# Optimization experiments

Hardware: AMD Instinct MI355X
Metric: run time of the kernel (lower is better)

Reference implementation:

```python
import jax, jax.numpy as jnp
import numpy as np

B, CIN, COUT, K = 32, 64, 64, 128  # batch, in_channels, out_channels, kernel_size (== H == W)


def setup_inputs() -> dict:
    key = jax.random.key(0)
    k1, k2, k3, k4 = jax.random.split(key, 4)
    x = jax.random.normal(k1, (B, CIN, K, K), dtype=jnp.float32)
    # kaiming_uniform_(a=sqrt(5)) => gain=sqrt(1/3), bound = gain*sqrt(3/fan_in) = 1/sqrt(fan_in)
    fan_in = CIN * K * K
    bound = 1.0 / np.sqrt(fan_in)
    weight_real = jax.random.uniform(k2, (COUT, CIN, K, K), jnp.float32, -bound, bound)
    weight_imag = jax.random.uniform(k3, (COUT, CIN, K, K), jnp.float32, -bound, bound)
    bias = jax.random.uniform(k4, (COUT,), jnp.float32, -bound, bound)
    return {"x": x, "weight_real": weight_real, "weight_imag": weight_imag, "bias": bias}


def reference(x, weight_real, weight_imag, bias):
    # FFT over spatial dims: (B, Cin, H, W) complex
    xf = jnp.fft.fftn(x, axes=(-2, -1))
    xr, xi = jnp.real(xf), jnp.imag(xf)
    # Per-frequency complex contraction over in-channels:
    # (a+ib)(c+id) = (ac - bd) + i(ad + bc)
    conv_real = (jnp.einsum('bchw,ochw->bohw', xr, weight_real)
                 - jnp.einsum('bchw,ochw->bohw', xi, weight_imag))
    conv_imag = (jnp.einsum('bchw,ochw->bohw', xr, weight_imag)
                 + jnp.einsum('bchw,ochw->bohw', xi, weight_real))
    conv = jnp.fft.ifftn(jax.lax.complex(conv_real, conv_imag), axes=(-2, -1))
    out = jnp.real(conv) + bias[:, None, None]
    return jax.nn.relu(out)
```

## Files before the change

### kernel.cpp

```cpp
#include <hip/hip_runtime.h>
#include <hip/hip_bf16.h>
#include <math.h>


#define PI2 6.28318530717958647692f
typedef unsigned int uint32;

__device__ __forceinline__ float2 cmulf(float2 a, float2 b) {
  return make_float2(a.x * b.x - a.y * b.y, a.x * b.y + a.y * b.x);
}
__device__ __forceinline__ uint32 pack_bf(float re, float im) {
  __hip_bfloat162 h;
  h.x = __float2bfloat16(re);
  h.y = __float2bfloat16(im);
  return *(uint32*)&h;
}
__device__ __forceinline__ float2 unpack_bf(uint32 v) {
  return make_float2(__uint_as_float(v << 16), __uint_as_float(v & 0xFFFF0000u));
}
__device__ __forceinline__ int br7(int i) { return __brev((unsigned)i) >> 25; }

template <int SGN>
__device__ __forceinline__ void wave_fft128(float2& e0, float2& e1, int l) {
#pragma unroll
  for (int s = 1; s <= 6; s++) {
    const int h = 1 << (s - 1);
    const int p = l & (h - 1);
    float sn, cs;
    __sincosf((float)SGN * PI2 * (float)p / (float)(2 * h), &sn, &cs);
    const float2 w = make_float2(cs, sn);
    const bool up = (l & h) != 0;
    const float2 o0 = make_float2(__shfl_xor(e0.x, h), __shfl_xor(e0.y, h));
    const float2 o1 = make_float2(__shfl_xor(e1.x, h), __shfl_xor(e1.y, h));
    const float2 u0 = up ? o0 : e0;
    const float2 m0 = up ? e0 : o0;
    const float2 u1 = up ? o1 : e1;
    const float2 m1 = up ? e1 : o1;
    const float2 t0 = cmulf(w, m0);
    const float2 t1 = cmulf(w, m1);
    e0 = up ? make_float2(u0.x - t0.x, u0.y - t0.y) : make_float2(u0.x + t0.x, u0.y + t0.y);
    e1 = up ? make_float2(u1.x - t1.x, u1.y - t1.y) : make_float2(u1.x + t1.x, u1.y + t1.y);
  }
  float sn, cs;
  __sincosf((float)SGN * PI2 * (float)l * (1.0f / 128.0f), &sn, &cs);
  const float2 w = make_float2(cs, sn);
  const float2 t = cmulf(w, e1);
  const float2 u = e0;
  e0 = make_float2(u.x + t.x, u.y + t.y);
  e1 = make_float2(u.x - t.x, u.y - t.y);
}

__global__ __launch_bounds__(256) void k_fft_rows(const float* __restrict__ x,
                                                  uint32* __restrict__ xf) {
  const int t = threadIdx.x, l = t & 63, wv = t >> 6;
  const int row = blockIdx.x * 4 + wv;
  const float* rp = x + (size_t)row * 128;
  const int brl = br7(l);
  const float2 v = *(const float2*)(rp + brl);
  float2 e0 = make_float2(v.x, 0.f);
  float2 e1 = make_float2(v.y, 0.f);
  wave_fft128<-1>(e0, e1, l);
  uint32* op = xf + (size_t)row * 128;
  op[l] = pack_bf(e0.x, e0.y);
  op[l + 64] = pack_bf(e1.x, e1.y);
}

__global__ __launch_bounds__(256) void k_fft_cols(uint32* __restrict__ buf, float sign) {
  __shared__ float2 tw[64];
  __shared__ float2 tile[128][33];
  const int t = threadIdx.x;
  if (t < 64) {
    float s, c;
    sincosf(sign * PI2 * (float)t * (1.0f / 128.0f), &s, &c);
    tw[t] = make_float2(c, s);
  }
  const int img = blockIdx.x >> 2;
  const int w0 = (blockIdx.x & 3) * 32;
  uint32* base = buf + img * 16384 + w0;
  const int j = t & 31, hh = t >> 5;
#pragma unroll
  for (int it = 0; it < 16; it++) {
    const int h = it * 8 + hh;
    tile[br7(h)][j] = unpack_bf(base[h * 128 + j]);
  }
  __syncthreads();
#pragma unroll
  for (int s = 0; s < 7; s++) {
    const int half = 1 << s;
#pragma unroll
    for (int kk = 0; kk < 8; kk++) {
      const int k = kk * 8 + hh;
      const int p = k & (half - 1);
      const int i0 = ((k >> s) << (s + 1)) + p;
      const int i1 = i0 + half;
      const float2 w = tw[p << (6 - s)];
      const float2 u = tile[i0][j];
      const float2 v = tile[i1][j];
      const float2 wv = cmulf(w, v);
      tile[i0][j] = make_float2(u.x + wv.x, u.y + wv.y);
      tile[i1][j] = make_float2(u.x - wv.x, u.y - wv.y);
    }
    __syncthreads();
  }
#pragma unroll
  for (int it = 0; it < 16; it++) {
    const int h = it * 8 + hh;
    base[h * 128 + j] = pack_bf(tile[h][j].x, tile[h][j].y);
  }
}

__global__ __launch_bounds__(256) void k_cgemm(const uint32* __restrict__ xf,
                                               const float* __restrict__ wr,
                                               const float* __restrict__ wi,
                                               uint32* __restrict__ y) {
  __shared__ uint32 xs[2][4096];
  const int t = threadIdx.x;
  const int fc = blockIdx.x >> 2, oq = blockIdx.x & 3;
  const int f0 = fc * 16;
  const int fl = t & 15;
  const int og = (t >> 4) & 3;
  const int bw = t >> 6;
  const int o0 = oq * 16 + og * 4;
  const int b0 = bw * 8;
  const int l = t & 63;
  const int lr = l >> 2, fq = l & 3;

  float2 acc[8][4] = {};

  auto stage = [&](int ci, int d) {
#pragma unroll
    for (int q = 0; q < 4; q++) {
      const int r = q * 64 + bw * 16 + lr;
      const int cc = r >> 5, b = r & 31;
      const uint32* gp = xf + ((unsigned)(b * 64 + ci * 8 + cc) * 16384u +
                               (unsigned)(f0 + fq * 4));
      uint32* lp = &xs[d][(q * 64 + bw * 16) * 16];
      __builtin_amdgcn_global_load_lds(
          (const __attribute__((address_space(1))) unsigned int*)gp,
          (__attribute__((address_space(3))) unsigned int*)lp, 16, 0, 0);
    }
  };

  stage(0, 0);
  for (int ci = 0; ci < 8; ci++) {
    __syncthreads();
    if (ci < 7) stage(ci + 1, (ci + 1) & 1);
    const int d = ci & 1;
    const int c0 = ci * 8;
#pragma unroll 2
    for (int cc = 0; cc < 8; cc++) {
      const int c = c0 + cc;
      const unsigned wbase = (unsigned)(o0 * 64 + c) * 16384u + (unsigned)(f0 + fl);
      float wr4[4], wi4[4];
#pragma unroll
      for (int jo = 0; jo < 4; jo++) {
        wr4[jo] = wr[wbase + (unsigned)jo * 1048576u];
        wi4[jo] = wi[wbase + (unsigned)jo * 1048576u];
      }
      float2 xv[8];
#pragma unroll
      for (int ib = 0; ib < 8; ib++)
        xv[ib] = unpack_bf(xs[d][(cc * 32 + b0 + ib) * 16 + fl]);
#pragma unroll
      for (int ib = 0; ib < 8; ib++) {
#pragma unroll
        for (int jo = 0; jo < 4; jo++) {
          acc[ib][jo].x = fmaf(xv[ib].x, wr4[jo], acc[ib][jo].x);
          acc[ib][jo].x = fmaf(-xv[ib].y, wi4[jo], acc[ib][jo].x);
          acc[ib][jo].y = fmaf(xv[ib].x, wi4[jo], acc[ib][jo].y);
          acc[ib][jo].y = fmaf(xv[ib].y, wr4[jo], acc[ib][jo].y);
        }
      }
    }
  }
#pragma unroll
  for (int ib = 0; ib < 8; ib++) {
#pragma unroll
    for (int jo = 0; jo < 4; jo++) {
      y[(unsigned)((b0 + ib) * 64 + o0 + jo) * 16384u + (unsigned)(f0 + fl)] =
          pack_bf(acc[ib][jo].x, acc[ib][jo].y);
    }
  }
}

__global__ __launch_bounds__(256) void k_ifft_rows_out(const uint32* __restrict__ y,
                                                       const float* __restrict__ bias,
                                                       float* __restrict__ out) {
  const int t = threadIdx.x, l = t & 63, wv = t >> 6;
  const int row = blockIdx.x * 4 + wv;
  const uint32* rp = y + (size_t)row * 128;
  const int brl = br7(l);
  const uint2 u = *(const uint2*)(rp + brl);
  float2 e0 = unpack_bf(u.x);
  float2 e1 = unpack_bf(u.y);
  wave_fft128<1>(e0, e1, l);
  const int o = (row >> 7) & 63;
  const float bb = bias[o];
  const float sc = 1.0f / 16384.0f;
  float* op = out + (size_t)row * 128;
  op[l] = fmaxf(fmaf(e0.x, sc, bb), 0.f);
  op[l + 64] = fmaxf(fmaf(e1.x, sc, bb), 0.f);
}

extern "C" void kernel_launch(void* const* d_in, const int* in_sizes, int n_in,
                              void* d_out, int out_size, void* d_ws, size_t ws_size,
                              hipStream_t stream) {
  const float* x = (const float*)d_in[0];
  const float* wr = (const float*)d_in[1];
  const float* wi = (const float*)d_in[2];
  const float* bias = (const float*)d_in[3];
  float* out = (float*)d_out;

  const size_t XF_BYTES = 134217728;
  if (ws_size < 2 * XF_BYTES) {
    hipMemsetAsync(d_out, 0, (size_t)out_size * sizeof(float), stream);
    return;
  }
  uint32* XF = (uint32*)d_ws;
  uint32* Y = (uint32*)((char*)d_ws + XF_BYTES);

  k_fft_rows<<<65536, 256, 0, stream>>>(x, XF);
  k_fft_cols<<<8192, 256, 0, stream>>>(XF, -1.0f);
  k_cgemm<<<4096, 256, 0, stream>>>(XF, wr, wi, Y);
  k_fft_cols<<<8192, 256, 0, stream>>>(Y, 1.0f);
  k_ifft_rows_out<<<65536, 256, 0, stream>>>(Y, bias, out);
}
```

Baseline: 1.210 ms.

## Retile complex GEMM so each block covers all out-channels and batches

The cgemm kernel now uses 512-thread blocks, each covering a 16-frequency chunk with all 64 output channels, so every x-spectrum tile is staged into LDS once rather than four times. Each thread now holds 32 batches by 2 output channels and prefetches its weight values one input channel ahead into registers. The aim is to cut redundant global reads of the transformed input and hide weight-load latency. The cost is 128 accumulator floats per thread, which raises register pressure and may limit occupancy, and a grid of only 1024 blocks.

```diff
diff --git a/kernel.cpp b/kernel.cpp
--- a/kernel.cpp
+++ b/kernel.cpp
@@ -109,77 +109,75 @@
   }
 }
 
-__global__ __launch_bounds__(256) void k_cgemm(const uint32* __restrict__ xf,
-                                               const float* __restrict__ wr,
-                                               const float* __restrict__ wi,
-                                               uint32* __restrict__ y) {
+__global__ __launch_bounds__(512, 2) void k_cgemm(const uint32* __restrict__ xf,
+                                                  const float* __restrict__ wr,
+                                                  const float* __restrict__ wi,
+                                                  uint32* __restrict__ y) {
   __shared__ uint32 xs[2][4096];
   const int t = threadIdx.x;
-  const int fc = blockIdx.x >> 2, oq = blockIdx.x & 3;
-  const int f0 = fc * 16;
+  const int f0 = blockIdx.x * 16;
   const int fl = t & 15;
-  const int og = (t >> 4) & 3;
-  const int bw = t >> 6;
-  const int o0 = oq * 16 + og * 4;
-  const int b0 = bw * 8;
-  const int l = t & 63;
-  const int lr = l >> 2, fq = l & 3;
-
-  float2 acc[8][4] = {};
+  const int grp = t >> 4;
+  const int o0 = grp * 2;
+  const int wv = t >> 6;
+
+  float2 acc[32][2] = {};
 
   auto stage = [&](int ci, int d) {
 #pragma unroll
-    for (int q = 0; q < 4; q++) {
-      const int r = q * 64 + bw * 16 + lr;
+    for (int q = 0; q < 2; q++) {
+      const int s = q * 512 + t;
+      const int r = s >> 2, fq = s & 3;
       const int cc = r >> 5, b = r & 31;
-      const uint32* gp = xf + ((unsigned)(b * 64 + ci * 8 + cc) * 16384u +
-                               (unsigned)(f0 + fq * 4));
-      uint32* lp = &xs[d][(q * 64 + bw * 16) * 16];
+      const uint32* gp = xf + (size_t)(b * 64 + ci * 8 + cc) * 16384u +
+                         (unsigned)(f0 + fq * 4);
+      uint32* lp = &xs[d][(unsigned)(q * 512 + wv * 64) * 4u];
       __builtin_amdgcn_global_load_lds(
           (const __attribute__((address_space(1))) unsigned int*)gp,
           (__attribute__((address_space(3))) unsigned int*)lp, 16, 0, 0);
     }
   };
 
+  const float* wrp = wr + (size_t)o0 * 64 * 16384 + (unsigned)(f0 + fl);
+  const float* wip = wi + (size_t)o0 * 64 * 16384 + (unsigned)(f0 + fl);
+
   stage(0, 0);
+  float w0r = wrp[0], w1r = wrp[(size_t)64 * 16384];
+  float w0i = wip[0], w1i = wip[(size_t)64 * 16384];
+
   for (int ci = 0; ci < 8; ci++) {
     __syncthreads();
     if (ci < 7) stage(ci + 1, (ci + 1) & 1);
     const int d = ci & 1;
-    const int c0 = ci * 8;
 #pragma unroll 2
     for (int cc = 0; cc < 8; cc++) {
-      const int c = c0 + cc;
-      const unsigned wbase = (unsigned)(o0 * 64 + c) * 16384u + (unsigned)(f0 + fl);
-      float wr4[4], wi4[4];
-#pragma unroll
-      for (int jo = 0; jo < 4; jo++) {
-        wr4[jo] = wr[wbase + (unsigned)jo * 1048576u];
-        wi4[jo] = wi[wbase + (unsigned)jo * 1048576u];
-      }
-      float2 xv[8];
-#pragma unroll
-      for (int ib = 0; ib < 8; ib++)
-        xv[ib] = unpack_bf(xs[d][(cc * 32 + b0 + ib) * 16 + fl]);
-#pragma unroll
-      for (int ib = 0; ib < 8; ib++) {
-#pragma unroll
-        for (int jo = 0; jo < 4; jo++) {
-          acc[ib][jo].x = fmaf(xv[ib].x, wr4[jo], acc[ib][jo].x);
-          acc[ib][jo].x = fmaf(-xv[ib].y, wi4[jo], acc[ib][jo].x);
-          acc[ib][jo].y = fmaf(xv[ib].x, wi4[jo], acc[ib][jo].y);
-          acc[ib][jo].y = fmaf(xv[ib].y, wr4[jo], acc[ib][jo].y);
-        }
+      const int c = ci * 8 + cc;
+      const float a0r = w0r, a1r = w1r, a0i = w0i, a1i = w1i;
+      const int cn = (c < 63) ? c + 1 : 63;
+      w0r = wrp[(size_t)cn * 16384];
+      w1r = wrp[(size_t)(64 + cn) * 16384];
+      w0i = wip[(size_t)cn * 16384];
+      w1i = wip[(size_t)(64 + cn) * 16384];
+#pragma unroll
+      for (int b = 0; b < 32; b++) {
+        const float2 xv = unpack_bf(xs[d][(cc * 32 + b) * 16 + fl]);
+        acc[b][0].x = fmaf(xv.x, a0r, acc[b][0].x);
+        acc[b][0].x = fmaf(-xv.y, a0i, acc[b][0].x);
+        acc[b][0].y = fmaf(xv.x, a0i, acc[b][0].y);
+        acc[b][0].y = fmaf(xv.y, a0r, acc[b][0].y);
+        acc[b][1].x = fmaf(xv.x, a1r, acc[b][1].x);
+        acc[b][1].x = fmaf(-xv.y, a1i, acc[b][1].x);
+        acc[b][1].y = fmaf(xv.x, a1i, acc[b][1].y);
+        acc[b][1].y = fmaf(xv.y, a1r, acc[b][1].y);
       }
     }
   }
 #pragma unroll
-  for (int ib = 0; ib < 8; ib++) {
-#pragma unroll
-    for (int jo = 0; jo < 4; jo++) {
-      y[(unsigned)((b0 + ib) * 64 + o0 + jo) * 16384u + (unsigned)(f0 + fl)] =
-          pack_bf(acc[ib][jo].x, acc[ib][jo].y);
-    }
+  for (int b = 0; b < 32; b++) {
+    y[(size_t)(b * 64 + o0) * 16384u + (unsigned)(f0 + fl)] =
+        pack_bf(acc[b][0].x, acc[b][0].y);
+    y[(size_t)(b * 64 + o0 + 1) * 16384u + (unsigned)(f0 + fl)] =
+        pack_bf(acc[b][1].x, acc[b][1].y);
   }
 }
 
@@ -221,7 +219,7 @@
 
   k_fft_rows<<<65536, 256, 0, stream>>>(x, XF);
   k_fft_cols<<<8192, 256, 0, stream>>>(XF, -1.0f);
-  k_cgemm<<<4096, 256, 0, stream>>>(XF, wr, wi, Y);
+  k_cgemm<<<1024, 512, 0, stream>>>(XF, wr, wi, Y);
   k_fft_cols<<<8192, 256, 0, stream>>>(Y, 1.0f);
   k_ifft_rows_out<<<65536, 256, 0, stream>>>(Y, bias, out);
 }
```

Result: faster. 1.106 ms (-8.6%).

## Merge output-channel quarters into 1024-thread cgemm blocks and prefetch weights

Applied to the files above, without the earlier changes.

The complex GEMM now runs one 1024-thread block per 16-frequency chunk covering all 64 output channels, where it used to launch four 256-thread blocks per chunk that each re-staged the same input tile. Each staged X tile in LDS is therefore shared by all output channels, which cuts redundant global/LDS staging by four. Weight loads are also software-prefetched one input channel ahead in registers to hide global latency. The cost is larger blocks, which may reduce scheduling flexibility and occupancy, plus extra register pressure from the prefetch.

```diff
diff --git a/kernel.cpp b/kernel.cpp
--- a/kernel.cpp
+++ b/kernel.cpp
@@ -109,66 +109,75 @@
   }
 }
 
-__global__ __launch_bounds__(256) void k_cgemm(const uint32* __restrict__ xf,
-                                               const float* __restrict__ wr,
-                                               const float* __restrict__ wi,
-                                               uint32* __restrict__ y) {
+__global__ __launch_bounds__(1024, 4) void k_cgemm(const uint32* __restrict__ xf,
+                                                   const float* __restrict__ wr,
+                                                   const float* __restrict__ wi,
+                                                   uint32* __restrict__ y) {
   __shared__ uint32 xs[2][4096];
   const int t = threadIdx.x;
-  const int fc = blockIdx.x >> 2, oq = blockIdx.x & 3;
-  const int f0 = fc * 16;
+  const int f0 = blockIdx.x * 16;
   const int fl = t & 15;
-  const int og = (t >> 4) & 3;
-  const int bw = t >> 6;
-  const int o0 = oq * 16 + og * 4;
-  const int b0 = bw * 8;
-  const int l = t & 63;
-  const int lr = l >> 2, fq = l & 3;
+  const int og = (t >> 4) & 15;
+  const int o0 = og * 4;
+  const int b0 = (t >> 8) * 8;
+  const int wv = t >> 6;
 
   float2 acc[8][4] = {};
 
   auto stage = [&](int ci, int d) {
-#pragma unroll
-    for (int q = 0; q < 4; q++) {
-      const int r = q * 64 + bw * 16 + lr;
-      const int cc = r >> 5, b = r & 31;
-      const uint32* gp = xf + ((unsigned)(b * 64 + ci * 8 + cc) * 16384u +
-                               (unsigned)(f0 + fq * 4));
-      uint32* lp = &xs[d][(q * 64 + bw * 16) * 16];
-      __builtin_amdgcn_global_load_lds(
-          (const __attribute__((address_space(1))) unsigned int*)gp,
-          (__attribute__((address_space(3))) unsigned int*)lp, 16, 0, 0);
-    }
+    const int r = t >> 2, fq = t & 3;
+    const int cc = r >> 5, b = r & 31;
+    const uint32* gp = xf + (size_t)(b * 64 + ci * 8 + cc) * 16384u +
+                       (unsigned)(f0 + fq * 4);
+    uint32* lp = &xs[d][(unsigned)wv * 256u];
+    __builtin_amdgcn_global_load_lds(
+        (const __attribute__((address_space(1))) unsigned int*)gp,
+        (__attribute__((address_space(3))) unsigned int*)lp, 16, 0, 0);
   };
 
+  const float* wrp = wr + (size_t)o0 * 1048576u + (unsigned)(f0 + fl);
+  const float* wip = wi + (size_t)o0 * 1048576u + (unsigned)(f0 + fl);
+
   stage(0, 0);
+  float cr[4], cim[4];
+#pragma unroll
+  for (int jo = 0; jo < 4; jo++) {
+    cr[jo] = wrp[(size_t)jo * 1048576u];
+    cim[jo] = wip[(size_t)jo * 1048576u];
+  }
+
   for (int ci = 0; ci < 8; ci++) {
     __syncthreads();
     if (ci < 7) stage(ci + 1, (ci + 1) & 1);
     const int d = ci & 1;
-    const int c0 = ci * 8;
 #pragma unroll 2
     for (int cc = 0; cc < 8; cc++) {
-      const int c = c0 + cc;
-      const unsigned wbase = (unsigned)(o0 * 64 + c) * 16384u + (unsigned)(f0 + fl);
-      float wr4[4], wi4[4];
+      const int c = ci * 8 + cc;
+      float ar[4], ai[4];
 #pragma unroll
       for (int jo = 0; jo < 4; jo++) {
-        wr4[jo] = wr[wbase + (unsigned)jo * 1048576u];
-        wi4[jo] = wi[wbase + (unsigned)jo * 1048576u];
+        ar[jo] = cr[jo];
+        ai[jo] = cim[jo];
       }
-      float2 xv[8];
+      const int cn = (c < 63) ? c + 1 : 63;
+#pragma unroll
+      for (int jo = 0; jo < 4; jo++) {
+        cr[jo] = wrp[(size_t)jo * 1048576u + (size_t)cn * 16384u];
+        cim[jo] = wip[(size_t)jo * 1048576u + (size_t)cn * 16384u];
+      }
+      uint32 xraw[8];
 #pragma unroll
       for (int ib = 0; ib < 8; ib++)
-        xv[ib] = unpack_bf(xs[d][(cc * 32 + b0 + ib) * 16 + fl]);
+        xraw[ib] = xs[d][(cc * 32 + b0 + ib) * 16 + fl];
 #pragma unroll
       for (int ib = 0; ib < 8; ib++) {
+        const float2 xv = unpack_bf(xraw[ib]);
 #pragma unroll
         for (int jo = 0; jo < 4; jo++) {
-          acc[ib][jo].x = fmaf(xv[ib].x, wr4[jo], acc[ib][jo].x);
-          acc[ib][jo].x = fmaf(-xv[ib].y, wi4[jo], acc[ib][jo].x);
-          acc[ib][jo].y = fmaf(xv[ib].x, wi4[jo], acc[ib][jo].y);
-          acc[ib][jo].y = fmaf(xv[ib].y, wr4[jo], acc[ib][jo].y);
+          acc[ib][jo].x = fmaf(xv.x, ar[jo], acc[ib][jo].x);
+          acc[ib][jo].x = fmaf(-xv.y, ai[jo], acc[ib][jo].x);
+          acc[ib][jo].y = fmaf(xv.x, ai[jo], acc[ib][jo].y);
+          acc[ib][jo].y = fmaf(xv.y, ar[jo], acc[ib][jo].y);
         }
       }
     }
@@ -177,7 +186,7 @@
   for (int ib = 0; ib < 8; ib++) {
 #pragma unroll
     for (int jo = 0; jo < 4; jo++) {
-      y[(unsigned)((b0 + ib) * 64 + o0 + jo) * 16384u + (unsigned)(f0 + fl)] =
+      y[(size_t)((b0 + ib) * 64 + o0 + jo) * 16384u + (unsigned)(f0 + fl)] =
           pack_bf(acc[ib][jo].x, acc[ib][jo].y);
     }
   }
@@ -221,7 +230,7 @@
 
   k_fft_rows<<<65536, 256, 0, stream>>>(x, XF);
   k_fft_cols<<<8192, 256, 0, stream>>>(XF, -1.0f);
-  k_cgemm<<<4096, 256, 0, stream>>>(XF, wr, wi, Y);
+  k_cgemm<<<1024, 1024, 0, stream>>>(XF, wr, wi, Y);
   k_fft_cols<<<8192, 256, 0, stream>>>(Y, 1.0f);
   k_ifft_rows_out<<<65536, 256, 0, stream>>>(Y, bias, out);
 }
```

After: 1.356 ms. 12.1% more time.
